# Kernel tuning notes

Measured on AMD Instinct MI355X. Metric: run time of the kernel, lower is better.

Reference implementation:

```python
import jax, jax.numpy as jnp
import numpy as np

HEADS = 8
KS = 7
PAD = 3


def grouped_conv1x1(x, w):
    # x: (B, Cin, H, W), w: (heads, Cout/h, Cin/h) -> (B, Cout, H, W)
    B, Cin, H, W = x.shape
    g, co, ci = w.shape
    xg = x.reshape(B, g, ci, H, W)
    out = jnp.einsum('bgchw,goc->bgohw', xg, w)
    return out.reshape(B, g * co, H, W)


def unfold2d(p, k):
    # p: (B, C, Hp, Wp) -> (B, C, H, W, k, k) sliding windows, stride 1
    B, C, Hp, Wp = p.shape
    H, W = Hp - k + 1, Wp - k + 1
    rows = [jnp.stack([p[:, :, i:i + H, j:j + W] for j in range(k)], axis=-1)
            for i in range(k)]
    return jnp.stack(rows, axis=-2)  # (B,C,H,W,k,k)


def setup_inputs() -> dict:
    key = jax.random.key(0)
    ks = jax.random.split(key, 7)
    B, Cin, H, W = 8, 64, 64, 64
    Cout = 64
    g = HEADS
    return {
        'x': jax.random.normal(ks[0], (B, Cin, H, W), jnp.float32),
        'r': jax.random.normal(ks[1], (1,), jnp.float32),
        'w_q': jax.random.normal(ks[2], (g, Cout // g, Cin // g), jnp.float32) * 0.2,
        'w_k': jax.random.normal(ks[3], (g, Cout // g, Cin // g), jnp.float32) * 0.2,
        'w_v': jax.random.normal(ks[4], (g, Cout // g, Cin // g), jnp.float32) * 0.2,
        'rel_h': jax.random.normal(ks[5], (Cout // 2, KS), jnp.float32),
        'rel_w': jax.random.normal(ks[6], (Cout // 2, KS), jnp.float32),
    }


def reference(x, r, w_q, w_k, w_v, rel_h, rel_w):
    B, Cin, H, W = x.shape
    g = HEADS
    Cout = w_q.shape[0] * w_q.shape[1]
    dh = Cout // g

    padded = jnp.pad(x, ((0, 0), (0, 0), (PAD, PAD), (PAD, PAD)))
    q = grouped_conv1x1(x, w_q)            # (B, Cout, H, W)
    k = grouped_conv1x1(padded, w_k)       # (B, Cout, H+2p, W+2p)
    v = grouped_conv1x1(padded, w_v)

    k = unfold2d(k, KS)                    # (B, Cout, H, W, KS, KS)
    v = unfold2d(v, KS)

    # learnable relative positional encoding: split channels in half,
    # add rel_h along window-height, rel_w along window-width
    half = Cout // 2
    k_h = k[:, :half] + rel_h[None, :, None, None, :, None]
    k_w = k[:, half:] + rel_w[None, :, None, None, None, :]
    k = jnp.concatenate([k_h, k_w], axis=1)

    K2 = KS * KS
    k = k.reshape(B, g, dh, H, W, K2)
    v = v.reshape(B, g, dh, H, W, K2)
    q = q.reshape(B, g, dh, H, W, 1)

    scale = np.sqrt(g / Cout).astype(np.float32)
    logits = (q * k).sum(axis=2, keepdims=True) * scale   # (B,g,1,H,W,K2)
    attn = jax.nn.softmax(logits, axis=-1)
    out = (attn * v).sum(axis=-1)                          # (B,g,dh,H,W)
    return out.reshape(B, Cout, H, W)
```

## Files before the change

kernel.cpp:

```cpp
#include <hip/hip_runtime.h>

#define NG  8
#define DH  8
#define KS  7
#define PAD 3
#define TH  16
#define TW  32
#define OW  2
#define TPH 22
#define TPW 38
#define LST 40
#define CH  64
#define HH  64
#define WW  64

__device__ __forceinline__ int imin(int a, int b) { return a < b ? a : b; }
__device__ __forceinline__ int imax(int a, int b) { return a > b ? a : b; }

__global__ __launch_bounds__(256, 1)
void saconv_kernel(const float* __restrict__ x,
                   const float* __restrict__ wq,
                   const float* __restrict__ wk,
                   const float* __restrict__ wv,
                   const float* __restrict__ relh,
                   const float* __restrict__ relw,
                   float* __restrict__ out) {
  __shared__ float xs[DH][TPH * LST];
  __shared__ float swq[DH * DH];
  __shared__ float swk[DH * DH];
  __shared__ float swv[DH * DH];
  __shared__ float srel[DH * KS];

  const int tx  = threadIdx.x;
  const int ty  = threadIdx.y;
  const int tid = ty * 16 + tx;
  const int bz  = blockIdx.z;
  const int b   = bz >> 3;
  const int g   = bz & 7;
  const int h0  = blockIdx.y * TH;
  const int w0  = blockIdx.x * TW;

  if (tid < DH * DH) swq[tid] = wq[g * DH * DH + tid];
  else if (tid < 2 * DH * DH) swk[tid - 64] = wk[g * DH * DH + tid - 64];
  else if (tid < 3 * DH * DH) swv[tid - 128] = wv[g * DH * DH + tid - 128];
  else if (tid < 3 * DH * DH + DH * KS) {
    int t2 = tid - 192;
    int c = t2 / KS, t = t2 - c * KS;
    int gc = g * DH + c;
    srel[t2] = (g < 4) ? relh[gc * KS + t] : relw[(gc - 32) * KS + t];
  }

  const float* xb = x + (size_t)(b * CH + g * DH) * (HH * WW);
  const int NF4 = DH * TPH * (LST / 4);
  #pragma unroll
  for (int kk = 0; kk < 7; kk++) {
    int f = tid + kk * 256;
    if (f < NF4) {
      int ci  = f / (TPH * 10);
      int r   = f - ci * (TPH * 10);
      int row = r / 10;
      int c4  = r - row * 10;
      int yy  = h0 + row - PAD;
      int cy  = imin(imax(yy, 0), HH - 1);
      bool yok = (yy >= 0) & (yy < HH);
      float v[4];
      #pragma unroll
      for (int e = 0; e < 4; e++) {
        int xx = w0 + 4 * c4 + e - PAD;
        int cx = imin(imax(xx, 0), WW - 1);
        bool inb = yok & (xx >= 0) & (xx < WW);
        float t = xb[(ci * HH + cy) * WW + cx];
        v[e] = inb ? t : 0.0f;
      }
      *(float4*)(&xs[ci][row * LST + 4 * c4]) = make_float4(v[0], v[1], v[2], v[3]);
    }
  }
  __syncthreads();

  const float scale = 0.35355339059327373f;
  float qk[OW][DH];
  float rq[OW][KS];
  {
    float q_[OW][DH];
    #pragma unroll
    for (int o = 0; o < OW; o++) {
      float xc[DH];
      #pragma unroll
      for (int ci = 0; ci < DH; ci++)
        xc[ci] = xs[ci][(ty + PAD) * LST + 2 * tx + o + PAD];
      #pragma unroll
      for (int c = 0; c < DH; c++) {
        float a = 0.f;
        #pragma unroll
        for (int ci = 0; ci < DH; ci++)
          a = fmaf(swq[c * DH + ci], xc[ci], a);
        q_[o][c] = a;
      }
    }
    #pragma unroll
    for (int o = 0; o < OW; o++)
      #pragma unroll
      for (int ci = 0; ci < DH; ci++) {
        float a = 0.f;
        #pragma unroll
        for (int c = 0; c < DH; c++)
          a = fmaf(q_[o][c], swk[c * DH + ci], a);
        qk[o][ci] = a * scale;
      }
    #pragma unroll
    for (int o = 0; o < OW; o++)
      #pragma unroll
      for (int t = 0; t < KS; t++) {
        float a = 0.f;
        #pragma unroll
        for (int c = 0; c < DH; c++)
          a = fmaf(q_[o][c], srel[c * KS + t], a);
        rq[o][t] = a * scale;
      }
  }

  const bool useI = (g < 4);

  float s[OW], xa[OW][DH];
  #pragma unroll
  for (int o = 0; o < OW; o++) {
    s[o] = 0.f;
    #pragma unroll
    for (int ci = 0; ci < DH; ci++) xa[o][ci] = 0.f;
  }

  #pragma unroll
  for (int i = 0; i < KS; i++) {
    const int rowoff = (ty + i) * LST + 2 * tx;
    float xr[DH][8];
    #pragma unroll
    for (int ci = 0; ci < DH; ci++) {
      const float* bp = &xs[ci][rowoff];
      float2 a0 = *(const float2*)(bp);
      float2 a1 = *(const float2*)(bp + 2);
      float2 a2 = *(const float2*)(bp + 4);
      float2 a3 = *(const float2*)(bp + 6);
      xr[ci][0] = a0.x; xr[ci][1] = a0.y; xr[ci][2] = a1.x; xr[ci][3] = a1.y;
      xr[ci][4] = a2.x; xr[ci][5] = a2.y; xr[ci][6] = a3.x; xr[ci][7] = a3.y;
    }

    #pragma unroll
    for (int o = 0; o < OW; o++) {
      float e[KS];
      float se = 0.f;
      #pragma unroll
      for (int j = 0; j < KS; j++) {
        float d = useI ? rq[o][i] : rq[o][j];
        #pragma unroll
        for (int ci = 0; ci < DH; ci++)
          d = fmaf(qk[o][ci], xr[ci][o + j], d);
        e[j] = __expf(d);
        se += e[j];
      }
      s[o] += se;
      #pragma unroll
      for (int ci = 0; ci < DH; ci++) {
        float a = xa[o][ci];
        #pragma unroll
        for (int j = 0; j < KS; j++)
          a = fmaf(e[j], xr[ci][o + j], a);
        xa[o][ci] = a;
      }
    }
  }

  #pragma unroll
  for (int o = 0; o < OW; o++) {
    float inv = 1.0f / s[o];
    #pragma unroll
    for (int ci = 0; ci < DH; ci++) xa[o][ci] *= inv;
  }

  const int h = h0 + ty;
  const int wbase = w0 + 2 * tx;
  #pragma unroll
  for (int c = 0; c < DH; c++) {
    float2 v2;
    {
      float a0 = 0.f, a1 = 0.f;
      #pragma unroll
      for (int ci = 0; ci < DH; ci++) {
        a0 = fmaf(swv[c * DH + ci], xa[0][ci], a0);
        a1 = fmaf(swv[c * DH + ci], xa[1][ci], a1);
      }
      v2.x = a0; v2.y = a1;
    }
    *(float2*)(&out[((size_t)(b * CH + g * DH + c) * HH + h) * WW + wbase]) = v2;
  }
}

extern "C" void kernel_launch(void* const* d_in, const int* in_sizes, int n_in,
                              void* d_out, int out_size, void* d_ws, size_t ws_size,
                              hipStream_t stream) {
  const float* x    = (const float*)d_in[0];
  const float* wq   = (const float*)d_in[2];
  const float* wk   = (const float*)d_in[3];
  const float* wv   = (const float*)d_in[4];
  const float* relh = (const float*)d_in[5];
  const float* relw = (const float*)d_in[6];
  float* out = (float*)d_out;

  const int B = in_sizes[0] / (CH * HH * WW);
  dim3 grid(WW / TW, HH / TH, B * NG);
  dim3 block(16, 16, 1);
  saconv_kernel<<<grid, block, 0, stream>>>(x, wq, wk, wv, relh, relw, out);
}
```

Baseline: 20.83 us.

## Split head channels across thread pairs with shuffle reductions and smaller tiles

Each thread now handles only half of the eight head channels, and partial logits and output projections are combined with cross-lane shuffles. The tile width is halved so there are twice as many blocks, and launch bounds allow four blocks per CU. The aim is more parallelism and lower register pressure in place of the single heavy block per CU. In exchange it duplicates the exp/softmax work on both halves, adds shuffles for every window row, and raises the halo overhead from smaller tiles.

```diff
diff --git a/kernel.cpp b/kernel.cpp
--- a/kernel.cpp
+++ b/kernel.cpp
@@ -2,14 +2,16 @@
 
 #define NG  8
 #define DH  8
+#define DHH 4
 #define KS  7
 #define PAD 3
 #define TH  16
-#define TW  32
+#define TW  16
 #define OW  2
 #define TPH 22
-#define TPW 38
-#define LST 40
+#define TPW 22
+#define LST 24
+#define PLANE 532
 #define CH  64
 #define HH  64
 #define WW  64
@@ -17,7 +19,7 @@
 __device__ __forceinline__ int imin(int a, int b) { return a < b ? a : b; }
 __device__ __forceinline__ int imax(int a, int b) { return a > b ? a : b; }
 
-__global__ __launch_bounds__(256, 1)
+__global__ __launch_bounds__(256, 4)
 void saconv_kernel(const float* __restrict__ x,
                    const float* __restrict__ wq,
                    const float* __restrict__ wk,
@@ -25,15 +27,16 @@
                    const float* __restrict__ relh,
                    const float* __restrict__ relw,
                    float* __restrict__ out) {
-  __shared__ float xs[DH][TPH * LST];
+  __shared__ float xs[DH * PLANE];
   __shared__ float swq[DH * DH];
   __shared__ float swk[DH * DH];
   __shared__ float swv[DH * DH];
   __shared__ float srel[DH * KS];
 
   const int tx  = threadIdx.x;
-  const int ty  = threadIdx.y;
-  const int tid = ty * 16 + tx;
+  const int tz  = threadIdx.y;
+  const int ty  = threadIdx.z;
+  const int tid = tx + 8 * tz + 16 * ty;
   const int bz  = blockIdx.z;
   const int b   = bz >> 3;
   const int g   = bz & 7;
@@ -51,15 +54,15 @@
   }
 
   const float* xb = x + (size_t)(b * CH + g * DH) * (HH * WW);
-  const int NF4 = DH * TPH * (LST / 4);
-  #pragma unroll
-  for (int kk = 0; kk < 7; kk++) {
+  const int NF4 = DH * TPH * 6;
+  #pragma unroll
+  for (int kk = 0; kk < 5; kk++) {
     int f = tid + kk * 256;
     if (f < NF4) {
-      int ci  = f / (TPH * 10);
-      int r   = f - ci * (TPH * 10);
-      int row = r / 10;
-      int c4  = r - row * 10;
+      int ci  = f / (TPH * 6);
+      int r   = f - ci * (TPH * 6);
+      int row = r / 6;
+      int c4  = r - row * 6;
       int yy  = h0 + row - PAD;
       int cy  = imin(imax(yy, 0), HH - 1);
       bool yok = (yy >= 0) & (yy < HH);
@@ -72,13 +75,14 @@
         float t = xb[(ci * HH + cy) * WW + cx];
         v[e] = inb ? t : 0.0f;
       }
-      *(float4*)(&xs[ci][row * LST + 4 * c4]) = make_float4(v[0], v[1], v[2], v[3]);
+      *(float4*)(&xs[ci * PLANE + row * LST + 4 * c4]) = make_float4(v[0], v[1], v[2], v[3]);
     }
   }
   __syncthreads();
 
   const float scale = 0.35355339059327373f;
-  float qk[OW][DH];
+  const int ci0 = 4 * tz;
+  float qk[OW][DHH];
   float rq[OW][KS];
   {
     float q_[OW][DH];
@@ -87,7 +91,7 @@
       float xc[DH];
       #pragma unroll
       for (int ci = 0; ci < DH; ci++)
-        xc[ci] = xs[ci][(ty + PAD) * LST + 2 * tx + o + PAD];
+        xc[ci] = xs[ci * PLANE + (ty + PAD) * LST + 2 * tx + o + PAD];
       #pragma unroll
       for (int c = 0; c < DH; c++) {
         float a = 0.f;
@@ -100,12 +104,12 @@
     #pragma unroll
     for (int o = 0; o < OW; o++)
       #pragma unroll
-      for (int ci = 0; ci < DH; ci++) {
+      for (int n = 0; n < DHH; n++) {
         float a = 0.f;
         #pragma unroll
         for (int c = 0; c < DH; c++)
-          a = fmaf(q_[o][c], swk[c * DH + ci], a);
-        qk[o][ci] = a * scale;
+          a = fmaf(q_[o][c], swk[c * DH + ci0 + n], a);
+        qk[o][n] = a * scale;
       }
     #pragma unroll
     for (int o = 0; o < OW; o++)
@@ -115,56 +119,68 @@
         #pragma unroll
         for (int c = 0; c < DH; c++)
           a = fmaf(q_[o][c], srel[c * KS + t], a);
-        rq[o][t] = a * scale;
+        rq[o][t] = a * (0.5f * scale);
       }
   }
 
   const bool useI = (g < 4);
 
-  float s[OW], xa[OW][DH];
+  float s[OW], xa[OW][DHH];
   #pragma unroll
   for (int o = 0; o < OW; o++) {
     s[o] = 0.f;
     #pragma unroll
-    for (int ci = 0; ci < DH; ci++) xa[o][ci] = 0.f;
-  }
+    for (int n = 0; n < DHH; n++) xa[o][n] = 0.f;
+  }
+
+  const float* xpl = xs + ci0 * PLANE;
 
   #pragma unroll
   for (int i = 0; i < KS; i++) {
     const int rowoff = (ty + i) * LST + 2 * tx;
-    float xr[DH][8];
-    #pragma unroll
-    for (int ci = 0; ci < DH; ci++) {
-      const float* bp = &xs[ci][rowoff];
+    float xr[DHH][8];
+    #pragma unroll
+    for (int n = 0; n < DHH; n++) {
+      const float* bp = xpl + n * PLANE + rowoff;
       float2 a0 = *(const float2*)(bp);
       float2 a1 = *(const float2*)(bp + 2);
       float2 a2 = *(const float2*)(bp + 4);
       float2 a3 = *(const float2*)(bp + 6);
-      xr[ci][0] = a0.x; xr[ci][1] = a0.y; xr[ci][2] = a1.x; xr[ci][3] = a1.y;
-      xr[ci][4] = a2.x; xr[ci][5] = a2.y; xr[ci][6] = a3.x; xr[ci][7] = a3.y;
-    }
+      xr[n][0] = a0.x; xr[n][1] = a0.y; xr[n][2] = a1.x; xr[n][3] = a1.y;
+      xr[n][4] = a2.x; xr[n][5] = a2.y; xr[n][6] = a3.x; xr[n][7] = a3.y;
+    }
+
+    float d[OW][KS];
+    #pragma unroll
+    for (int o = 0; o < OW; o++)
+      #pragma unroll
+      for (int j = 0; j < KS; j++) {
+        float a = useI ? rq[o][i] : rq[o][j];
+        #pragma unroll
+        for (int n = 0; n < DHH; n++)
+          a = fmaf(qk[o][n], xr[n][o + j], a);
+        d[o][j] = a;
+      }
+
+    #pragma unroll
+    for (int o = 0; o < OW; o++)
+      #pragma unroll
+      for (int j = 0; j < KS; j++)
+        d[o][j] += __shfl_xor(d[o][j], 8, 64);
 
     #pragma unroll
     for (int o = 0; o < OW; o++) {
-      float e[KS];
-      float se = 0.f;
-      #pragma unroll
-      for (int j = 0; j < KS; j++) {
-        float d = useI ? rq[o][i] : rq[o][j];
-        #pragma unroll
-        for (int ci = 0; ci < DH; ci++)
-          d = fmaf(qk[o][ci], xr[ci][o + j], d);
-        e[j] = __expf(d);
-        se += e[j];
-      }
+      float e[KS], se = 0.f;
+      #pragma unroll
+      for (int j = 0; j < KS; j++) { e[j] = __expf(d[o][j]); se += e[j]; }
       s[o] += se;
       #pragma unroll
-      for (int ci = 0; ci < DH; ci++) {
-        float a = xa[o][ci];
+      for (int n = 0; n < DHH; n++) {
+        float a = xa[o][n];
         #pragma unroll
         for (int j = 0; j < KS; j++)
-          a = fmaf(e[j], xr[ci][o + j], a);
-        xa[o][ci] = a;
+          a = fmaf(e[j], xr[n][o + j], a);
+        xa[o][n] = a;
       }
     }
   }
@@ -173,24 +189,33 @@
   for (int o = 0; o < OW; o++) {
     float inv = 1.0f / s[o];
     #pragma unroll
-    for (int ci = 0; ci < DH; ci++) xa[o][ci] *= inv;
-  }
+    for (int n = 0; n < DHH; n++) xa[o][n] *= inv;
+  }
+
+  const int cio = 4 - ci0;
+  float po_own[OW][DHH], po_oth[OW][DHH];
+  #pragma unroll
+  for (int o = 0; o < OW; o++)
+    #pragma unroll
+    for (int n = 0; n < DHH; n++) {
+      float a0 = 0.f, a1 = 0.f;
+      #pragma unroll
+      for (int m = 0; m < DHH; m++) {
+        a0 = fmaf(swv[(ci0 + n) * DH + ci0 + m], xa[o][m], a0);
+        a1 = fmaf(swv[(cio + n) * DH + ci0 + m], xa[o][m], a1);
+      }
+      po_own[o][n] = a0;
+      po_oth[o][n] = a1;
+    }
 
   const int h = h0 + ty;
   const int wbase = w0 + 2 * tx;
   #pragma unroll
-  for (int c = 0; c < DH; c++) {
+  for (int n = 0; n < DHH; n++) {
     float2 v2;
-    {
-      float a0 = 0.f, a1 = 0.f;
-      #pragma unroll
-      for (int ci = 0; ci < DH; ci++) {
-        a0 = fmaf(swv[c * DH + ci], xa[0][ci], a0);
-        a1 = fmaf(swv[c * DH + ci], xa[1][ci], a1);
-      }
-      v2.x = a0; v2.y = a1;
-    }
-    *(float2*)(&out[((size_t)(b * CH + g * DH + c) * HH + h) * WW + wbase]) = v2;
+    v2.x = po_own[0][n] + __shfl_xor(po_oth[0][n], 8, 64);
+    v2.y = po_own[1][n] + __shfl_xor(po_oth[1][n], 8, 64);
+    *(float2*)(&out[((size_t)(b * CH + g * DH + ci0 + n) * HH + h) * WW + wbase]) = v2;
   }
 }
 
@@ -207,6 +232,6 @@
 
   const int B = in_sizes[0] / (CH * HH * WW);
   dim3 grid(WW / TW, HH / TH, B * NG);
-  dim3 block(16, 16, 1);
+  dim3 block(8, 2, 16);
   saconv_kernel<<<grid, block, 0, stream>>>(x, wq, wk, wv, relh, relw, out);
 }
```

New measurement: 34.99 us. +67.9%, slower.

## Split window rows across two threads with fp16 channel-paired LDS tile

Applied to the files above, without the earlier changes.

Doubles the block to 512 threads, with each pixel pair now handled by two threads. Each thread processes half of the 7 window rows, and the partial softmax sums and weighted accumulators are combined with cross-lane shuffles. The shared-memory input tile is stored as packed fp16 channel pairs, which halves LDS footprint and read traffic, and the weights are read straight from global memory instead of being staged in LDS. This raises parallelism and occupancy, at the cost of fp16 rounding of the inputs, duplicated q/k projection work in both halves, and some idle lanes on the uneven row split.

```diff
diff --git a/kernel.cpp b/kernel.cpp
--- a/kernel.cpp
+++ b/kernel.cpp
@@ -6,18 +6,19 @@
 #define PAD 3
 #define TH  16
 #define TW  32
-#define OW  2
-#define TPH 22
-#define TPW 38
-#define LST 40
 #define CH  64
 #define HH  64
 #define WW  64
+#define RST 80
+#define PLH 1768
+
+typedef __fp16 h2 __attribute__((ext_vector_type(2)));
+typedef __fp16 h4 __attribute__((ext_vector_type(4)));
 
 __device__ __forceinline__ int imin(int a, int b) { return a < b ? a : b; }
 __device__ __forceinline__ int imax(int a, int b) { return a > b ? a : b; }
 
-__global__ __launch_bounds__(256, 1)
+__global__ __launch_bounds__(512, 4)
 void saconv_kernel(const float* __restrict__ x,
                    const float* __restrict__ wq,
                    const float* __restrict__ wk,
@@ -25,172 +26,175 @@
                    const float* __restrict__ relh,
                    const float* __restrict__ relw,
                    float* __restrict__ out) {
-  __shared__ float xs[DH][TPH * LST];
-  __shared__ float swq[DH * DH];
-  __shared__ float swk[DH * DH];
-  __shared__ float swv[DH * DH];
-  __shared__ float srel[DH * KS];
-
-  const int tx  = threadIdx.x;
-  const int ty  = threadIdx.y;
-  const int tid = ty * 16 + tx;
-  const int bz  = blockIdx.z;
-  const int b   = bz >> 3;
-  const int g   = bz & 7;
-  const int h0  = blockIdx.y * TH;
-  const int w0  = blockIdx.x * TW;
-
-  if (tid < DH * DH) swq[tid] = wq[g * DH * DH + tid];
-  else if (tid < 2 * DH * DH) swk[tid - 64] = wk[g * DH * DH + tid - 64];
-  else if (tid < 3 * DH * DH) swv[tid - 128] = wv[g * DH * DH + tid - 128];
-  else if (tid < 3 * DH * DH + DH * KS) {
-    int t2 = tid - 192;
-    int c = t2 / KS, t = t2 - c * KS;
-    int gc = g * DH + c;
-    srel[t2] = (g < 4) ? relh[gc * KS + t] : relw[(gc - 32) * KS + t];
-  }
+  __shared__ __fp16 xs[4 * PLH];
+
+  const int tx    = threadIdx.x;
+  const int ihalf = threadIdx.y;
+  const int ty    = threadIdx.z;
+  const int tid   = tx + 16 * ihalf + 32 * ty;
+  const int bz = blockIdx.z;
+  const int b  = bz >> 3;
+  const int g  = bz & 7;
+  const int h0 = blockIdx.y * TH;
+  const int w0 = blockIdx.x * TW;
 
   const float* xb = x + (size_t)(b * CH + g * DH) * (HH * WW);
-  const int NF4 = DH * TPH * (LST / 4);
   #pragma unroll
   for (int kk = 0; kk < 7; kk++) {
-    int f = tid + kk * 256;
-    if (f < NF4) {
-      int ci  = f / (TPH * 10);
-      int r   = f - ci * (TPH * 10);
-      int row = r / 10;
-      int c4  = r - row * 10;
-      int yy  = h0 + row - PAD;
-      int cy  = imin(imax(yy, 0), HH - 1);
-      bool yok = (yy >= 0) & (yy < HH);
-      float v[4];
-      #pragma unroll
-      for (int e = 0; e < 4; e++) {
-        int xx = w0 + 4 * c4 + e - PAD;
-        int cx = imin(imax(xx, 0), WW - 1);
-        bool inb = yok & (xx >= 0) & (xx < WW);
-        float t = xb[(ci * HH + cy) * WW + cx];
-        v[e] = inb ? t : 0.0f;
-      }
-      *(float4*)(&xs[ci][row * LST + 4 * c4]) = make_float4(v[0], v[1], v[2], v[3]);
+    int f = tid + kk * 512;
+    if (f < 3520) {
+      int cp  = f / 880;
+      int r   = f - cp * 880;
+      int row = r / 40;
+      int col = r - row * 40;
+      int yy = h0 + row - PAD;
+      int xx = w0 + col - PAD;
+      bool inb = (yy >= 0) & (yy < HH) & (xx >= 0) & (xx < WW);
+      int cy = imin(imax(yy, 0), HH - 1);
+      int cx = imin(imax(xx, 0), WW - 1);
+      const float* p0 = xb + ((size_t)(2 * cp) * HH + cy) * WW + cx;
+      float v0 = p0[0];
+      float v1 = p0[HH * WW];
+      if (!inb) { v0 = 0.f; v1 = 0.f; }
+      *(h2*)&xs[cp * PLH + row * RST + col * 2] = __builtin_amdgcn_cvt_pkrtz(v0, v1);
     }
   }
   __syncthreads();
 
   const float scale = 0.35355339059327373f;
-  float qk[OW][DH];
-  float rq[OW][KS];
+  float qk[2][DH];
+  float rq[2][8];
   {
-    float q_[OW][DH];
-    #pragma unroll
-    for (int o = 0; o < OW; o++) {
-      float xc[DH];
+    float xc[2][DH];
+    #pragma unroll
+    for (int o = 0; o < 2; o++)
       #pragma unroll
       for (int ci = 0; ci < DH; ci++)
-        xc[ci] = xs[ci][(ty + PAD) * LST + 2 * tx + o + PAD];
+        xc[o][ci] = (float)xs[(ci >> 1) * PLH + (ty + PAD) * RST
+                              + (2 * tx + o + PAD) * 2 + (ci & 1)];
+    float q_[2][DH];
+    #pragma unroll
+    for (int o = 0; o < 2; o++)
       #pragma unroll
       for (int c = 0; c < DH; c++) {
         float a = 0.f;
         #pragma unroll
         for (int ci = 0; ci < DH; ci++)
-          a = fmaf(swq[c * DH + ci], xc[ci], a);
+          a = fmaf(wq[(g * DH + c) * DH + ci], xc[o][ci], a);
         q_[o][c] = a;
       }
-    }
-    #pragma unroll
-    for (int o = 0; o < OW; o++)
+    #pragma unroll
+    for (int o = 0; o < 2; o++)
       #pragma unroll
       for (int ci = 0; ci < DH; ci++) {
         float a = 0.f;
         #pragma unroll
         for (int c = 0; c < DH; c++)
-          a = fmaf(q_[o][c], swk[c * DH + ci], a);
+          a = fmaf(q_[o][c], wk[(g * DH + c) * DH + ci], a);
         qk[o][ci] = a * scale;
       }
     #pragma unroll
-    for (int o = 0; o < OW; o++)
+    for (int o = 0; o < 2; o++)
       #pragma unroll
       for (int t = 0; t < KS; t++) {
         float a = 0.f;
         #pragma unroll
-        for (int c = 0; c < DH; c++)
-          a = fmaf(q_[o][c], srel[c * KS + t], a);
+        for (int c = 0; c < DH; c++) {
+          float rv = (g < 4) ? relh[(g * DH + c) * KS + t]
+                             : relw[((g - 4) * DH + c) * KS + t];
+          a = fmaf(q_[o][c], rv, a);
+        }
         rq[o][t] = a * scale;
       }
+    rq[0][7] = 0.f; rq[1][7] = 0.f;
   }
 
   const bool useI = (g < 4);
-
-  float s[OW], xa[OW][DH];
-  #pragma unroll
-  for (int o = 0; o < OW; o++) {
-    s[o] = 0.f;
+  float s[2] = {0.f, 0.f};
+  float xa[2][DH];
+  #pragma unroll
+  for (int o = 0; o < 2; o++)
     #pragma unroll
     for (int ci = 0; ci < DH; ci++) xa[o][ci] = 0.f;
-  }
-
-  #pragma unroll
-  for (int i = 0; i < KS; i++) {
-    const int rowoff = (ty + i) * LST + 2 * tx;
-    float xr[DH][8];
+
+  #pragma unroll
+  for (int u = 0; u < 4; u++) {
+    if (u + 4 * ihalf < KS) {
+      const int row = ty + 4 * ihalf + u;
+      h4 xr[4][4];
+      #pragma unroll
+      for (int cp = 0; cp < 4; cp++) {
+        const h4* rp = (const h4*)&xs[cp * PLH + row * RST + 4 * tx];
+        xr[cp][0] = rp[0]; xr[cp][1] = rp[1]; xr[cp][2] = rp[2]; xr[cp][3] = rp[3];
+      }
+      #pragma unroll
+      for (int o = 0; o < 2; o++) {
+        float e[KS], se = 0.f;
+        #pragma unroll
+        for (int j = 0; j < KS; j++) {
+          float d = useI ? (ihalf ? rq[o][imin(4 + u, 7)] : rq[o][u]) : rq[o][j];
+          #pragma unroll
+          for (int ci = 0; ci < DH; ci++) {
+            const int t = o + j;
+            d = fmaf((float)xr[ci >> 1][t >> 1][((t & 1) << 1) | (ci & 1)],
+                     qk[o][ci], d);
+          }
+          e[j] = __expf(d);
+          se += e[j];
+        }
+        s[o] += se;
+        #pragma unroll
+        for (int ci = 0; ci < DH; ci++) {
+          float a = xa[o][ci];
+          #pragma unroll
+          for (int j = 0; j < KS; j++) {
+            const int t = o + j;
+            a = fmaf(e[j], (float)xr[ci >> 1][t >> 1][((t & 1) << 1) | (ci & 1)], a);
+          }
+          xa[o][ci] = a;
+        }
+      }
+    }
+  }
+
+  float xav[2][DH];
+  float inv[2];
+  #pragma unroll
+  for (int o = 0; o < 2; o++) {
+    float st = s[o] + __shfl_xor(s[o], 16, 64);
+    inv[o] = 1.0f / st;
+  }
+  #pragma unroll
+  for (int o = 0; o < 2; o++)
     #pragma unroll
     for (int ci = 0; ci < DH; ci++) {
-      const float* bp = &xs[ci][rowoff];
-      float2 a0 = *(const float2*)(bp);
-      float2 a1 = *(const float2*)(bp + 2);
-      float2 a2 = *(const float2*)(bp + 4);
-      float2 a3 = *(const float2*)(bp + 6);
-      xr[ci][0] = a0.x; xr[ci][1] = a0.y; xr[ci][2] = a1.x; xr[ci][3] = a1.y;
-      xr[ci][4] = a2.x; xr[ci][5] = a2.y; xr[ci][6] = a3.x; xr[ci][7] = a3.y;
-    }
-
-    #pragma unroll
-    for (int o = 0; o < OW; o++) {
-      float e[KS];
-      float se = 0.f;
-      #pragma unroll
-      for (int j = 0; j < KS; j++) {
-        float d = useI ? rq[o][i] : rq[o][j];
-        #pragma unroll
-        for (int ci = 0; ci < DH; ci++)
-          d = fmaf(qk[o][ci], xr[ci][o + j], d);
-        e[j] = __expf(d);
-        se += e[j];
-      }
-      s[o] += se;
-      #pragma unroll
-      for (int ci = 0; ci < DH; ci++) {
-        float a = xa[o][ci];
-        #pragma unroll
-        for (int j = 0; j < KS; j++)
-          a = fmaf(e[j], xr[ci][o + j], a);
-        xa[o][ci] = a;
-      }
-    }
-  }
-
-  #pragma unroll
-  for (int o = 0; o < OW; o++) {
-    float inv = 1.0f / s[o];
-    #pragma unroll
-    for (int ci = 0; ci < DH; ci++) xa[o][ci] *= inv;
-  }
+      float t_ = xa[o][ci];
+      xav[o][ci] = (t_ + __shfl_xor(t_, 16, 64)) * inv[o];
+    }
+
+  float ov[2][DH];
+  #pragma unroll
+  for (int o = 0; o < 2; o++)
+    #pragma unroll
+    for (int c = 0; c < DH; c++) {
+      float a = 0.f;
+      #pragma unroll
+      for (int ci = 0; ci < DH; ci++)
+        a = fmaf(wv[(g * DH + c) * DH + ci], xav[o][ci], a);
+      ov[o][c] = a;
+    }
 
   const int h = h0 + ty;
-  const int wbase = w0 + 2 * tx;
-  #pragma unroll
-  for (int c = 0; c < DH; c++) {
-    float2 v2;
-    {
-      float a0 = 0.f, a1 = 0.f;
-      #pragma unroll
-      for (int ci = 0; ci < DH; ci++) {
-        a0 = fmaf(swv[c * DH + ci], xa[0][ci], a0);
-        a1 = fmaf(swv[c * DH + ci], xa[1][ci], a1);
-      }
-      v2.x = a0; v2.y = a1;
-    }
-    *(float2*)(&out[((size_t)(b * CH + g * DH + c) * HH + h) * WW + wbase]) = v2;
+  const int wb = w0 + 2 * tx;
+  float* ob = out + (((size_t)(b * CH + g * DH) * HH + h) * WW + wb);
+  if (ihalf == 0) {
+    #pragma unroll
+    for (int n = 0; n < 4; n++)
+      *(float2*)(ob + (size_t)n * (HH * WW)) = make_float2(ov[0][n], ov[1][n]);
+  } else {
+    #pragma unroll
+    for (int n = 0; n < 4; n++)
+      *(float2*)(ob + (size_t)(4 + n) * (HH * WW)) = make_float2(ov[0][4 + n], ov[1][4 + n]);
   }
 }
 
@@ -207,6 +211,6 @@
 
   const int B = in_sizes[0] / (CH * HH * WW);
   dim3 grid(WW / TW, HH / TH, B * NG);
-  dim3 block(16, 16, 1);
+  dim3 block(16, 2, 16);
   saconv_kernel<<<grid, block, 0, stream>>>(x, wq, wk, wv, relh, relw, out);
 }
```

Result: slower. 34.55 us (+65.8%).

## Store input tile as packed fp16 channel pairs and use fdot2 for logits

Applied to the files above, without the earlier changes.

Converts the shared-memory input tile from fp32 per-channel planes to packed half2 channel pairs. The logit dot product uses the v_dot2 fp16 instruction, and exp is replaced by exp2 with log2(e) folded into the scale. This halves LDS footprint and read traffic and halves the FMA count in the logit loop. In exchange it loses input precision to fp16 (round-toward-zero) and adds fp16-to-fp32 conversions in the value accumulation.

```diff
diff --git a/kernel.cpp b/kernel.cpp
--- a/kernel.cpp
+++ b/kernel.cpp
@@ -1,18 +1,23 @@
 #include <hip/hip_runtime.h>
+#include <math.h>
 
 #define NG  8
 #define DH  8
+#define NCP 4
 #define KS  7
 #define PAD 3
 #define TH  16
 #define TW  32
 #define OW  2
 #define TPH 22
-#define TPW 38
-#define LST 40
+#define RSTW 40
+#define PLW  (TPH * RSTW)
 #define CH  64
 #define HH  64
 #define WW  64
+
+typedef __fp16 h2v __attribute__((ext_vector_type(2)));
+typedef __fp16 h4v __attribute__((ext_vector_type(4)));
 
 __device__ __forceinline__ int imin(int a, int b) { return a < b ? a : b; }
 __device__ __forceinline__ int imax(int a, int b) { return a > b ? a : b; }
@@ -25,7 +30,7 @@
                    const float* __restrict__ relh,
                    const float* __restrict__ relw,
                    float* __restrict__ out) {
-  __shared__ float xs[DH][TPH * LST];
+  __shared__ h2v xs2[NCP * PLW];
   __shared__ float swq[DH * DH];
   __shared__ float swk[DH * DH];
   __shared__ float swv[DH * DH];
@@ -51,61 +56,74 @@
   }
 
   const float* xb = x + (size_t)(b * CH + g * DH) * (HH * WW);
-  const int NF4 = DH * TPH * (LST / 4);
+  const int NCHK = NCP * TPH * 19;
   #pragma unroll
   for (int kk = 0; kk < 7; kk++) {
     int f = tid + kk * 256;
-    if (f < NF4) {
-      int ci  = f / (TPH * 10);
-      int r   = f - ci * (TPH * 10);
-      int row = r / 10;
-      int c4  = r - row * 10;
+    if (f < NCHK) {
+      int cp  = f / (TPH * 19);
+      int r   = f - cp * (TPH * 19);
+      int row = r / 19;
+      int cc  = r - row * 19;
       int yy  = h0 + row - PAD;
       int cy  = imin(imax(yy, 0), HH - 1);
       bool yok = (yy >= 0) & (yy < HH);
-      float v[4];
-      #pragma unroll
-      for (int e = 0; e < 4; e++) {
-        int xx = w0 + 4 * c4 + e - PAD;
+      const float* p0 = xb + ((size_t)(2 * cp) * HH + cy) * WW;
+      float v0[2], v1[2];
+      #pragma unroll
+      for (int e = 0; e < 2; e++) {
+        int xx = w0 + 2 * cc + e - PAD;
         int cx = imin(imax(xx, 0), WW - 1);
         bool inb = yok & (xx >= 0) & (xx < WW);
-        float t = xb[(ci * HH + cy) * WW + cx];
-        v[e] = inb ? t : 0.0f;
-      }
-      *(float4*)(&xs[ci][row * LST + 4 * c4]) = make_float4(v[0], v[1], v[2], v[3]);
+        float a0 = p0[cx];
+        float a1 = p0[HH * WW + cx];
+        v0[e] = inb ? a0 : 0.0f;
+        v1[e] = inb ? a1 : 0.0f;
+      }
+      h2v pk0 = __builtin_amdgcn_cvt_pkrtz(v0[0], v1[0]);
+      h2v pk1 = __builtin_amdgcn_cvt_pkrtz(v0[1], v1[1]);
+      h4v w4 = { pk0.x, pk0.y, pk1.x, pk1.y };
+      *(h4v*)&xs2[cp * PLW + row * RSTW + 2 * cc] = w4;
     }
   }
   __syncthreads();
 
   const float scale = 0.35355339059327373f;
-  float qk[OW][DH];
+  const float L2E   = 1.4426950408889634f;
+  h2v  qkh[OW][NCP];
   float rq[OW][KS];
   {
+    float xc[OW][DH];
+    #pragma unroll
+    for (int o = 0; o < OW; o++)
+      #pragma unroll
+      for (int cp = 0; cp < NCP; cp++) {
+        h2v wv2 = xs2[cp * PLW + (ty + PAD) * RSTW + (2 * tx + o + PAD)];
+        xc[o][2 * cp]     = (float)wv2.x;
+        xc[o][2 * cp + 1] = (float)wv2.y;
+      }
     float q_[OW][DH];
     #pragma unroll
-    for (int o = 0; o < OW; o++) {
-      float xc[DH];
-      #pragma unroll
-      for (int ci = 0; ci < DH; ci++)
-        xc[ci] = xs[ci][(ty + PAD) * LST + 2 * tx + o + PAD];
+    for (int o = 0; o < OW; o++)
       #pragma unroll
       for (int c = 0; c < DH; c++) {
         float a = 0.f;
         #pragma unroll
         for (int ci = 0; ci < DH; ci++)
-          a = fmaf(swq[c * DH + ci], xc[ci], a);
+          a = fmaf(swq[c * DH + ci], xc[o][ci], a);
         q_[o][c] = a;
       }
-    }
-    #pragma unroll
-    for (int o = 0; o < OW; o++)
-      #pragma unroll
-      for (int ci = 0; ci < DH; ci++) {
-        float a = 0.f;
-        #pragma unroll
-        for (int c = 0; c < DH; c++)
-          a = fmaf(q_[o][c], swk[c * DH + ci], a);
-        qk[o][ci] = a * scale;
+    #pragma unroll
+    for (int o = 0; o < OW; o++)
+      #pragma unroll
+      for (int cp = 0; cp < NCP; cp++) {
+        float a0 = 0.f, a1 = 0.f;
+        #pragma unroll
+        for (int c = 0; c < DH; c++) {
+          a0 = fmaf(q_[o][c], swk[c * DH + 2 * cp], a0);
+          a1 = fmaf(q_[o][c], swk[c * DH + 2 * cp + 1], a1);
+        }
+        qkh[o][cp] = __builtin_amdgcn_cvt_pkrtz(a0 * (scale * L2E), a1 * (scale * L2E));
       }
     #pragma unroll
     for (int o = 0; o < OW; o++)
@@ -115,7 +133,7 @@
         #pragma unroll
         for (int c = 0; c < DH; c++)
           a = fmaf(q_[o][c], srel[c * KS + t], a);
-        rq[o][t] = a * scale;
+        rq[o][t] = a * (scale * L2E);
       }
   }
 
@@ -131,17 +149,20 @@
 
   #pragma unroll
   for (int i = 0; i < KS; i++) {
-    const int rowoff = (ty + i) * LST + 2 * tx;
-    float xr[DH][8];
-    #pragma unroll
-    for (int ci = 0; ci < DH; ci++) {
-      const float* bp = &xs[ci][rowoff];
-      float2 a0 = *(const float2*)(bp);
-      float2 a1 = *(const float2*)(bp + 2);
-      float2 a2 = *(const float2*)(bp + 4);
-      float2 a3 = *(const float2*)(bp + 6);
-      xr[ci][0] = a0.x; xr[ci][1] = a0.y; xr[ci][2] = a1.x; xr[ci][3] = a1.y;
-      xr[ci][4] = a2.x; xr[ci][5] = a2.y; xr[ci][6] = a3.x; xr[ci][7] = a3.y;
+    const int wbase = (ty + i) * RSTW + 2 * tx;
+    h2v xw[NCP][8];
+    #pragma unroll
+    for (int cp = 0; cp < NCP; cp++) {
+      const h4v* bp = (const h4v*)&xs2[cp * PLW + wbase];
+      h4v r0 = bp[0], r1 = bp[1], r2 = bp[2], r3 = bp[3];
+      xw[cp][0] = __builtin_shufflevector(r0, r0, 0, 1);
+      xw[cp][1] = __builtin_shufflevector(r0, r0, 2, 3);
+      xw[cp][2] = __builtin_shufflevector(r1, r1, 0, 1);
+      xw[cp][3] = __builtin_shufflevector(r1, r1, 2, 3);
+      xw[cp][4] = __builtin_shufflevector(r2, r2, 0, 1);
+      xw[cp][5] = __builtin_shufflevector(r2, r2, 2, 3);
+      xw[cp][6] = __builtin_shufflevector(r3, r3, 0, 1);
+      xw[cp][7] = __builtin_shufflevector(r3, r3, 2, 3);
     }
 
     #pragma unroll
@@ -152,19 +173,23 @@
       for (int j = 0; j < KS; j++) {
         float d = useI ? rq[o][i] : rq[o][j];
         #pragma unroll
-        for (int ci = 0; ci < DH; ci++)
-          d = fmaf(qk[o][ci], xr[ci][o + j], d);
-        e[j] = __expf(d);
+        for (int cp = 0; cp < NCP; cp++)
+          d = __builtin_amdgcn_fdot2(qkh[o][cp], xw[cp][o + j], d, false);
+        e[j] = exp2f(d);
         se += e[j];
       }
       s[o] += se;
       #pragma unroll
-      for (int ci = 0; ci < DH; ci++) {
-        float a = xa[o][ci];
-        #pragma unroll
-        for (int j = 0; j < KS; j++)
-          a = fmaf(e[j], xr[ci][o + j], a);
-        xa[o][ci] = a;
+      for (int cp = 0; cp < NCP; cp++) {
+        float a0 = xa[o][2 * cp];
+        float a1 = xa[o][2 * cp + 1];
+        #pragma unroll
+        for (int j = 0; j < KS; j++) {
+          a0 = fmaf(e[j], (float)xw[cp][o + j].x, a0);
+          a1 = fmaf(e[j], (float)xw[cp][o + j].y, a1);
+        }
+        xa[o][2 * cp]     = a0;
+        xa[o][2 * cp + 1] = a1;
       }
     }
   }
```

Result: faster. 19.67 us (-5.6%).
